# Performance work log

Hardware: AMD Instinct MI355X
Metric: run time of the kernel (lower is better)

Reference implementation:

```python
import jax, jax.numpy as jnp
import numpy as np

ALPHA = 1.0
EPS = 1e-12  # tf.nn.l2_normalize epsilon


def setup_inputs() -> dict:
    key = jax.random.key(0)
    k1, k2 = jax.random.split(key)
    B, I, J, D, K = 32, 32, 32, 128, 64
    features = jax.random.normal(k1, (B, I, J, D), dtype=jnp.float32)
    kmeans_centers = jax.random.normal(k2, (B, K, D), dtype=jnp.float32)
    return {"features": features, "kmeans_centers": kmeans_centers}


def reference(features, kmeans_centers):
    # features: (B, I, J, D); kmeans_centers: (B, K, D)
    B = features.shape[0]
    # Squared distance ||f - c||^2 expanded to avoid materializing (B,I,J,K,D)
    f2 = jnp.sum(features * features, axis=-1)[..., None]          # (B,I,J,1)
    c2 = jnp.sum(kmeans_centers * kmeans_centers, axis=-1)[:, None, None, :]  # (B,1,1,K)
    fc = jnp.einsum('bijd,bkd->bijk', features, kmeans_centers)     # (B,I,J,K)
    d2 = f2 - 2.0 * fc + c2                                         # (B,I,J,K)
    sim = jax.nn.softmax(-ALPHA * d2, axis=-1)                      # (B,I,J,K)
    # vlad[b,k,d] = sum_ij sim[b,i,j,k] * (f[b,i,j,d] - c[b,k,d])
    vlad = (jnp.einsum('bijk,bijd->bkd', sim, features)
            - jnp.sum(sim, axis=(1, 2))[..., None] * kmeans_centers)  # (B,K,D)
    flat = vlad.reshape(B, -1)                                      # (B, K*D)
    # K.l2_normalize with axis=None -> normalize over ALL elements (global norm)
    norm = jnp.sqrt(jnp.maximum(jnp.sum(flat * flat), EPS))
    return flat / norm
```

## Files before the change

kernel.cpp:

```cpp
#include <hip/hip_runtime.h>


#define NB    32
#define NIJ   1024
#define ND    128
#define NK    64
#define SPLIT 16
#define PPB   64

typedef short short8 __attribute__((ext_vector_type(8)));
typedef float f32x4  __attribute__((ext_vector_type(4)));

__device__ __forceinline__ float bf2f(unsigned short u) {
    return __uint_as_float(((unsigned)u) << 16);
}
__device__ __forceinline__ unsigned short f2bf(float f) {
    unsigned u = __float_as_uint(f);
    return (unsigned short)((u + 0x7fffu + ((u >> 16) & 1u)) >> 16);
}

__global__ __launch_bounds__(256, 2)
void netvlad_main(const float* __restrict__ feat,
                  const float* __restrict__ cent,
                  float* __restrict__ partial)
{
    __shared__ __align__(16) char smem[81920];
    ushort4* centHi = (ushort4*)smem;
    ushort4* centLo = (ushort4*)(smem + 16384);
    float4*  fL     = (float4*)(smem + 32768);
    float*   simf   = (float*)(smem + 65536);
    float4*  sim4   = (float4*)(smem + 65536);

    const int tid = threadIdx.x;
    const int bs  = blockIdx.x;
    const int b   = bs >> 4;
    const int n0  = (bs & 15) * PPB;

    const float4* cent4 = (const float4*)cent + (size_t)b * (NK * ND / 4);
    const float4* feat4 = (const float4*)feat + ((size_t)b * NIJ + n0) * (ND / 4);

    #pragma unroll
    for (int it = 0; it < 8; ++it) {
        int g  = it * 256 + tid;
        int k  = g >> 5;
        int d4 = g & 31;
        float4 v = cent4[g];
        ushort4 h, l;
        h.x = f2bf(v.x); l.x = f2bf(v.x - bf2f(h.x));
        h.y = f2bf(v.y); l.y = f2bf(v.y - bf2f(h.y));
        h.z = f2bf(v.z); l.z = f2bf(v.z - bf2f(h.z));
        h.w = f2bf(v.w); l.w = f2bf(v.w - bf2f(h.w));
        int idx = k * 32 + (d4 ^ ((k & 7) << 1));
        centHi[idx] = h; centLo[idx] = l;
    }
    #pragma unroll
    for (int it = 0; it < 8; ++it) {
        int g  = it * 256 + tid;
        int p  = g >> 5;
        int d4 = g & 31;
        fL[p * 32 + (d4 ^ (p & 7))] = feat4[g];
    }
    __syncthreads();

    if (tid < NK) {
        int k = tid;
        float a = 0.f;
        #pragma unroll
        for (int d4 = 0; d4 < 32; ++d4) {
            int idx = k * 32 + (d4 ^ ((k & 7) << 1));
            ushort4 h = centHi[idx], l = centLo[idx];
            float c0 = bf2f(h.x) + bf2f(l.x);
            float c1 = bf2f(h.y) + bf2f(l.y);
            float c2v = bf2f(h.z) + bf2f(l.z);
            float c3 = bf2f(h.w) + bf2f(l.w);
            a += c0 * c0 + c1 * c1 + c2v * c2v + c3 * c3;
        }
        simf[k] = a;
    }
    __syncthreads();

    const int w  = tid >> 6;
    const int l  = tid & 63;
    const int lr = l & 15;
    const int lg = l >> 4;

    float c2r[4];
    #pragma unroll
    for (int nt = 0; nt < 4; ++nt) c2r[nt] = simf[nt * 16 + lr];
    __syncthreads();

    f32x4 acc[4];
    #pragma unroll
    for (int nt = 0; nt < 4; ++nt) acc[nt] = (f32x4){0.f, 0.f, 0.f, 0.f};

    const int prow = 16 * w + lr;
    #pragma unroll
    for (int kt = 0; kt < 4; ++kt) {
        float4 fa = fL[prow * 32 + ((kt * 8 + 2 * lg + 0) ^ (prow & 7))];
        float4 fb = fL[prow * 32 + ((kt * 8 + 2 * lg + 1) ^ (prow & 7))];
        float fv[8] = { fa.x, fa.y, fa.z, fa.w, fb.x, fb.y, fb.z, fb.w };
        short8 ah, al;
        #pragma unroll
        for (int j = 0; j < 8; ++j) {
            unsigned short h = f2bf(fv[j]);
            ah[j] = (short)h;
            al[j] = (short)f2bf(fv[j] - bf2f(h));
        }
        #pragma unroll
        for (int nt = 0; nt < 4; ++nt) {
            int c  = nt * 16 + lr;
            int ch = c * 16 + ((kt * 4 + lg) ^ (c & 7));
            short8 bh = *(const short8*)(smem + ch * 16);
            short8 bl = *(const short8*)(smem + 16384 + ch * 16);
            acc[nt] = __builtin_amdgcn_mfma_f32_16x16x32_bf16(ah, bh, acc[nt], 0, 0, 0);
            acc[nt] = __builtin_amdgcn_mfma_f32_16x16x32_bf16(ah, bl, acc[nt], 0, 0, 0);
            acc[nt] = __builtin_amdgcn_mfma_f32_16x16x32_bf16(al, bh, acc[nt], 0, 0, 0);
        }
    }

    #pragma unroll
    for (int r = 0; r < 4; ++r) {
        float s[4];
        #pragma unroll
        for (int nt = 0; nt < 4; ++nt) s[nt] = 2.f * acc[nt][r] - c2r[nt];
        float m = fmaxf(fmaxf(s[0], s[1]), fmaxf(s[2], s[3]));
        #pragma unroll
        for (int o = 8; o >= 1; o >>= 1) m = fmaxf(m, __shfl_xor(m, o));
        float e[4], t = 0.f;
        #pragma unroll
        for (int nt = 0; nt < 4; ++nt) { e[nt] = __expf(s[nt] - m); t += e[nt]; }
        #pragma unroll
        for (int o = 8; o >= 1; o >>= 1) t += __shfl_xor(t, o);
        float inv = __builtin_amdgcn_rcpf(t);
        int p = 16 * w + 4 * lg + r;
        #pragma unroll
        for (int nt = 0; nt < 4; ++nt) {
            int k  = nt * 16 + lr;
            int kc = k >> 2;
            int slot = (((kc >> 2) ^ ((p >> 2) & 3)) << 2) | ((kc & 3) ^ (p & 3));
            simf[p * 64 + slot * 4 + (k & 3)] = e[nt] * inv;
        }
    }
    __syncthreads();

    const int kg = tid >> 5;
    const int dg = tid & 31;
    float4 a2[8];
    float  ss[8];
    #pragma unroll
    for (int i = 0; i < 8; ++i) { a2[i] = make_float4(0.f, 0.f, 0.f, 0.f); ss[i] = 0.f; }

    const int kcq = kg >> 1;
    const int kl0 = 2 * (kg & 1);
    #pragma unroll 4
    for (int p = 0; p < 64; ++p) {
        float4 fv = fL[p * 32 + (dg ^ (p & 7))];
        int pz2 = (p >> 2) & 3, pz = p & 3;
        int s0 = (((kcq ^ pz2) << 2) | ((kl0 + 0) ^ pz));
        int s1 = (((kcq ^ pz2) << 2) | ((kl0 + 1) ^ pz));
        float4 sa = sim4[p * 16 + s0];
        float4 sb = sim4[p * 16 + s1];
        float sv[8] = { sa.x, sa.y, sa.z, sa.w, sb.x, sb.y, sb.z, sb.w };
        #pragma unroll
        for (int i = 0; i < 8; ++i) {
            a2[i].x += sv[i] * fv.x;
            a2[i].y += sv[i] * fv.y;
            a2[i].z += sv[i] * fv.z;
            a2[i].w += sv[i] * fv.w;
            ss[i]   += sv[i];
        }
    }

    float4* out4 = (float4*)partial + (size_t)bs * (NK * ND / 4);
    #pragma unroll
    for (int i = 0; i < 8; ++i) {
        int k   = kg * 8 + i;
        int idx = k * 32 + (dg ^ ((k & 7) << 1));
        ushort4 h = centHi[idx], lo = centLo[idx];
        float4 o;
        o.x = a2[i].x - ss[i] * (bf2f(h.x) + bf2f(lo.x));
        o.y = a2[i].y - ss[i] * (bf2f(h.y) + bf2f(lo.y));
        o.z = a2[i].z - ss[i] * (bf2f(h.z) + bf2f(lo.z));
        o.w = a2[i].w - ss[i] * (bf2f(h.w) + bf2f(lo.w));
        out4[k * 32 + dg] = o;
    }
}

__global__ __launch_bounds__(256)
void netvlad_reduce(const float* __restrict__ partial,
                    float* __restrict__ vlad,
                    float* __restrict__ sqpart) {
    __shared__ float wsum[4];
    int idx = blockIdx.x * 256 + threadIdx.x;
    int b   = idx >> 11;
    int r   = idx & 2047;
    const float4* p4 = (const float4*)partial;
    float4 a = make_float4(0.f, 0.f, 0.f, 0.f);
    #pragma unroll
    for (int s = 0; s < SPLIT; ++s) {
        float4 v = p4[((size_t)(b * SPLIT + s)) * 2048 + r];
        a.x += v.x; a.y += v.y; a.z += v.z; a.w += v.w;
    }
    ((float4*)vlad)[idx] = a;
    float sq = a.x * a.x + a.y * a.y + a.z * a.z + a.w * a.w;
    #pragma unroll
    for (int o = 32; o >= 1; o >>= 1) sq += __shfl_xor(sq, o);
    if ((threadIdx.x & 63) == 0) wsum[threadIdx.x >> 6] = sq;
    __syncthreads();
    if (threadIdx.x == 0) sqpart[blockIdx.x] = wsum[0] + wsum[1] + wsum[2] + wsum[3];
}

__global__ __launch_bounds__(256)
void netvlad_norm(const float* __restrict__ vlad,
                  const float* __restrict__ sqpart,
                  float* __restrict__ out) {
    const float4* sq4 = (const float4*)sqpart;
    float4 v = sq4[threadIdx.x & 63];
    float t = v.x + v.y + v.z + v.w;
    #pragma unroll
    for (int o = 32; o >= 1; o >>= 1) t += __shfl_xor(t, o);
    float inv = __builtin_amdgcn_rcpf(sqrtf(fmaxf(t, 1e-12f)));
    int idx = blockIdx.x * 256 + threadIdx.x;
    float4 x = ((const float4*)vlad)[idx];
    float4 o4 = make_float4(x.x * inv, x.y * inv, x.z * inv, x.w * inv);
    ((float4*)out)[idx] = o4;
}

extern "C" void kernel_launch(void* const* d_in, const int* in_sizes, int n_in,
                              void* d_out, int out_size, void* d_ws, size_t ws_size,
                              hipStream_t stream) {
    const float* feat = (const float*)d_in[0];
    const float* cent = (const float*)d_in[1];
    float* out = (float*)d_out;

    char* ws = (char*)d_ws;
    const size_t partial_bytes = (size_t)NB * SPLIT * NK * ND * sizeof(float);
    const size_t vlad_bytes    = (size_t)NB * NK * ND * sizeof(float);
    float* partial = (float*)ws;
    float* vlad    = (float*)(ws + partial_bytes);
    float* sqpart  = (float*)(ws + partial_bytes + vlad_bytes);

    netvlad_main  <<<NB * SPLIT, 256, 0, stream>>>(feat, cent, partial);
    netvlad_reduce<<<256, 256, 0, stream>>>(partial, vlad, sqpart);
    netvlad_norm  <<<256, 256, 0, stream>>>(vlad, sqpart, out);
}
```

Measured before the change: 85.56 us.

## Compute VLAD aggregation with bf16 MFMA and move centre subtraction to reduce

The second contraction (sim^T × features) moves from scalar FP32 FMAs to bf16 MFMA, using transposed, swizzled bf16 copies of the features and similarities in LDS. Features are loaded straight from global into registers for the first MFMA instead of going through an FP32 LDS tile, which cuts shared memory to allow more occupancy. Per-split similarity sums are written to a new global buffer, and the reduce kernel subtracts ssum*centre. The cost is lower precision in the aggregation, since both operands are single bf16 with no hi/lo split.

```diff
diff --git a/kernel.cpp b/kernel.cpp
--- a/kernel.cpp
+++ b/kernel.cpp
@@ -2,11 +2,7 @@
 
 
 #define NB    32
-#define NIJ   1024
-#define ND    128
-#define NK    64
 #define SPLIT 16
-#define PPB   64
 
 typedef short short8 __attribute__((ext_vector_type(8)));
 typedef float f32x4  __attribute__((ext_vector_type(4)));
@@ -18,26 +14,29 @@
     unsigned u = __float_as_uint(f);
     return (unsigned short)((u + 0x7fffu + ((u >> 16) & 1u)) >> 16);
 }
+__device__ __forceinline__ int swz3(int x) { return (x ^ (x >> 3)) & 7; }
 
 __global__ __launch_bounds__(256, 2)
 void netvlad_main(const float* __restrict__ feat,
                   const float* __restrict__ cent,
-                  float* __restrict__ partial)
+                  float* __restrict__ partial,
+                  float* __restrict__ ssumG)
 {
-    __shared__ __align__(16) char smem[81920];
-    ushort4* centHi = (ushort4*)smem;
-    ushort4* centLo = (ushort4*)(smem + 16384);
-    float4*  fL     = (float4*)(smem + 32768);
-    float*   simf   = (float*)(smem + 65536);
-    float4*  sim4   = (float4*)(smem + 65536);
+    __shared__ __align__(16) char smem[58624];
+    ushort4*        centHi = (ushort4*)smem;
+    ushort4*        centLo = (ushort4*)(smem + 16384);
+    unsigned short* FT     = (unsigned short*)(smem + 32768);
+    unsigned short* ST     = (unsigned short*)(smem + 49152);
+    float*          c2L    = (float*)(smem + 57344);
+    float*          ssumW  = (float*)(smem + 57600);
 
     const int tid = threadIdx.x;
     const int bs  = blockIdx.x;
     const int b   = bs >> 4;
-    const int n0  = (bs & 15) * PPB;
-
-    const float4* cent4 = (const float4*)cent + (size_t)b * (NK * ND / 4);
-    const float4* feat4 = (const float4*)feat + ((size_t)b * NIJ + n0) * (ND / 4);
+    const int n0  = (bs & 15) * 64;
+
+    const float4* cent4 = (const float4*)cent + (size_t)b * 2048;
+    const float4* feat4 = (const float4*)feat + ((size_t)b * 1024 + n0) * 32;
 
     #pragma unroll
     for (int it = 0; it < 8; ++it) {
@@ -53,16 +52,31 @@
         int idx = k * 32 + (d4 ^ ((k & 7) << 1));
         centHi[idx] = h; centLo[idx] = l;
     }
-    #pragma unroll
-    for (int it = 0; it < 8; ++it) {
-        int g  = it * 256 + tid;
-        int p  = g >> 5;
-        int d4 = g & 31;
-        fL[p * 32 + (d4 ^ (p & 7))] = feat4[g];
-    }
-    __syncthreads();
-
-    if (tid < NK) {
+
+    const int w    = tid >> 6;
+    const int lane = tid & 63;
+    const int lr   = lane & 15;
+    const int lg   = lane >> 4;
+    const int prow = 16 * w + lr;
+
+    short8 ah[4], al[4];
+    #pragma unroll
+    for (int kt = 0; kt < 4; ++kt) {
+        float4 fa = feat4[prow * 32 + kt * 8 + 2 * lg + 0];
+        float4 fb = feat4[prow * 32 + kt * 8 + 2 * lg + 1];
+        float fv[8] = { fa.x, fa.y, fa.z, fa.w, fb.x, fb.y, fb.z, fb.w };
+        #pragma unroll
+        for (int j = 0; j < 8; ++j) {
+            unsigned short h = f2bf(fv[j]);
+            ah[kt][j] = (short)h;
+            al[kt][j] = (short)f2bf(fv[j] - bf2f(h));
+            int d = kt * 32 + 8 * lg + j;
+            FT[d * 64 + ((((prow >> 3) ^ swz3(d))) << 3) + (prow & 7)] = h;
+        }
+    }
+    __syncthreads();
+
+    if (tid < 64) {
         int k = tid;
         float a = 0.f;
         #pragma unroll
@@ -75,49 +89,32 @@
             float c3 = bf2f(h.w) + bf2f(l.w);
             a += c0 * c0 + c1 * c1 + c2v * c2v + c3 * c3;
         }
-        simf[k] = a;
-    }
-    __syncthreads();
-
-    const int w  = tid >> 6;
-    const int l  = tid & 63;
-    const int lr = l & 15;
-    const int lg = l >> 4;
+        c2L[k] = a;
+    }
+    __syncthreads();
 
     float c2r[4];
     #pragma unroll
-    for (int nt = 0; nt < 4; ++nt) c2r[nt] = simf[nt * 16 + lr];
-    __syncthreads();
+    for (int nt = 0; nt < 4; ++nt) c2r[nt] = c2L[nt * 16 + lr];
 
     f32x4 acc[4];
     #pragma unroll
     for (int nt = 0; nt < 4; ++nt) acc[nt] = (f32x4){0.f, 0.f, 0.f, 0.f};
-
-    const int prow = 16 * w + lr;
     #pragma unroll
     for (int kt = 0; kt < 4; ++kt) {
-        float4 fa = fL[prow * 32 + ((kt * 8 + 2 * lg + 0) ^ (prow & 7))];
-        float4 fb = fL[prow * 32 + ((kt * 8 + 2 * lg + 1) ^ (prow & 7))];
-        float fv[8] = { fa.x, fa.y, fa.z, fa.w, fb.x, fb.y, fb.z, fb.w };
-        short8 ah, al;
-        #pragma unroll
-        for (int j = 0; j < 8; ++j) {
-            unsigned short h = f2bf(fv[j]);
-            ah[j] = (short)h;
-            al[j] = (short)f2bf(fv[j] - bf2f(h));
-        }
         #pragma unroll
         for (int nt = 0; nt < 4; ++nt) {
             int c  = nt * 16 + lr;
             int ch = c * 16 + ((kt * 4 + lg) ^ (c & 7));
             short8 bh = *(const short8*)(smem + ch * 16);
             short8 bl = *(const short8*)(smem + 16384 + ch * 16);
-            acc[nt] = __builtin_amdgcn_mfma_f32_16x16x32_bf16(ah, bh, acc[nt], 0, 0, 0);
-            acc[nt] = __builtin_amdgcn_mfma_f32_16x16x32_bf16(ah, bl, acc[nt], 0, 0, 0);
-            acc[nt] = __builtin_amdgcn_mfma_f32_16x16x32_bf16(al, bh, acc[nt], 0, 0, 0);
-        }
-    }
-
+            acc[nt] = __builtin_amdgcn_mfma_f32_16x16x32_bf16(ah[kt], bh, acc[nt], 0, 0, 0);
+            acc[nt] = __builtin_amdgcn_mfma_f32_16x16x32_bf16(ah[kt], bl, acc[nt], 0, 0, 0);
+            acc[nt] = __builtin_amdgcn_mfma_f32_16x16x32_bf16(al[kt], bh, acc[nt], 0, 0, 0);
+        }
+    }
+
+    float ssp[4] = {0.f, 0.f, 0.f, 0.f};
     #pragma unroll
     for (int r = 0; r < 4; ++r) {
         float s[4];
@@ -135,72 +132,73 @@
         int p = 16 * w + 4 * lg + r;
         #pragma unroll
         for (int nt = 0; nt < 4; ++nt) {
-            int k  = nt * 16 + lr;
-            int kc = k >> 2;
-            int slot = (((kc >> 2) ^ ((p >> 2) & 3)) << 2) | ((kc & 3) ^ (p & 3));
-            simf[p * 64 + slot * 4 + (k & 3)] = e[nt] * inv;
-        }
-    }
-    __syncthreads();
-
-    const int kg = tid >> 5;
-    const int dg = tid & 31;
-    float4 a2[8];
-    float  ss[8];
-    #pragma unroll
-    for (int i = 0; i < 8; ++i) { a2[i] = make_float4(0.f, 0.f, 0.f, 0.f); ss[i] = 0.f; }
-
-    const int kcq = kg >> 1;
-    const int kl0 = 2 * (kg & 1);
-    #pragma unroll 4
-    for (int p = 0; p < 64; ++p) {
-        float4 fv = fL[p * 32 + (dg ^ (p & 7))];
-        int pz2 = (p >> 2) & 3, pz = p & 3;
-        int s0 = (((kcq ^ pz2) << 2) | ((kl0 + 0) ^ pz));
-        int s1 = (((kcq ^ pz2) << 2) | ((kl0 + 1) ^ pz));
-        float4 sa = sim4[p * 16 + s0];
-        float4 sb = sim4[p * 16 + s1];
-        float sv[8] = { sa.x, sa.y, sa.z, sa.w, sb.x, sb.y, sb.z, sb.w };
-        #pragma unroll
-        for (int i = 0; i < 8; ++i) {
-            a2[i].x += sv[i] * fv.x;
-            a2[i].y += sv[i] * fv.y;
-            a2[i].z += sv[i] * fv.z;
-            a2[i].w += sv[i] * fv.w;
-            ss[i]   += sv[i];
-        }
-    }
-
-    float4* out4 = (float4*)partial + (size_t)bs * (NK * ND / 4);
-    #pragma unroll
-    for (int i = 0; i < 8; ++i) {
-        int k   = kg * 8 + i;
-        int idx = k * 32 + (dg ^ ((k & 7) << 1));
-        ushort4 h = centHi[idx], lo = centLo[idx];
-        float4 o;
-        o.x = a2[i].x - ss[i] * (bf2f(h.x) + bf2f(lo.x));
-        o.y = a2[i].y - ss[i] * (bf2f(h.y) + bf2f(lo.y));
-        o.z = a2[i].z - ss[i] * (bf2f(h.z) + bf2f(lo.z));
-        o.w = a2[i].w - ss[i] * (bf2f(h.w) + bf2f(lo.w));
-        out4[k * 32 + dg] = o;
+            int k = nt * 16 + lr;
+            float val = e[nt] * inv;
+            ssp[nt] += val;
+            ST[k * 64 + ((((p >> 3) ^ swz3(k))) << 3) + (p & 7)] = f2bf(val);
+        }
+    }
+    #pragma unroll
+    for (int nt = 0; nt < 4; ++nt) {
+        float v = ssp[nt];
+        v += __shfl_xor(v, 16);
+        v += __shfl_xor(v, 32);
+        if (lg == 0) ssumW[w * 64 + nt * 16 + lr] = v;
+    }
+    __syncthreads();
+
+    if (tid < 64)
+        ssumG[bs * 64 + tid] = ssumW[tid] + ssumW[64 + tid] + ssumW[128 + tid] + ssumW[192 + tid];
+
+    f32x4 vac[8];
+    #pragma unroll
+    for (int dt = 0; dt < 8; ++dt) vac[dt] = (f32x4){0.f, 0.f, 0.f, 0.f};
+    const int krow = 16 * w + lr;
+    #pragma unroll
+    for (int ks = 0; ks < 2; ++ks) {
+        int cA = (ks * 4 + lg) ^ swz3(krow);
+        short8 af = *(const short8*)(ST + krow * 64 + (cA << 3));
+        #pragma unroll
+        for (int dt = 0; dt < 8; ++dt) {
+            int d  = dt * 16 + lr;
+            int cB = (ks * 4 + lg) ^ swz3(d);
+            short8 bf = *(const short8*)(FT + d * 64 + (cB << 3));
+            vac[dt] = __builtin_amdgcn_mfma_f32_16x16x32_bf16(af, bf, vac[dt], 0, 0, 0);
+        }
+    }
+
+    float* outp = partial + (size_t)bs * 8192;
+    #pragma unroll
+    for (int r = 0; r < 4; ++r) {
+        int k = 16 * w + 4 * lg + r;
+        #pragma unroll
+        for (int dt = 0; dt < 8; ++dt)
+            outp[k * 128 + dt * 16 + lr] = vac[dt][r];
     }
 }
 
 __global__ __launch_bounds__(256)
 void netvlad_reduce(const float* __restrict__ partial,
+                    const float* __restrict__ cent,
+                    const float* __restrict__ ssumG,
                     float* __restrict__ vlad,
                     float* __restrict__ sqpart) {
     __shared__ float wsum[4];
     int idx = blockIdx.x * 256 + threadIdx.x;
     int b   = idx >> 11;
-    int r   = idx & 2047;
+    int rem = idx & 2047;
+    int k   = rem >> 5;
     const float4* p4 = (const float4*)partial;
     float4 a = make_float4(0.f, 0.f, 0.f, 0.f);
+    float  ss = 0.f;
     #pragma unroll
     for (int s = 0; s < SPLIT; ++s) {
-        float4 v = p4[((size_t)(b * SPLIT + s)) * 2048 + r];
+        float4 v = p4[((size_t)(b * SPLIT + s)) * 2048 + rem];
         a.x += v.x; a.y += v.y; a.z += v.z; a.w += v.w;
-    }
+        ss += ssumG[(b * SPLIT + s) * 64 + k];
+    }
+    float4 c4 = ((const float4*)cent)[b * 2048 + rem];
+    a.x -= ss * c4.x; a.y -= ss * c4.y; a.z -= ss * c4.z; a.w -= ss * c4.w;
     ((float4*)vlad)[idx] = a;
     float sq = a.x * a.x + a.y * a.y + a.z * a.z + a.w * a.w;
     #pragma unroll
@@ -222,8 +220,7 @@
     float inv = __builtin_amdgcn_rcpf(sqrtf(fmaxf(t, 1e-12f)));
     int idx = blockIdx.x * 256 + threadIdx.x;
     float4 x = ((const float4*)vlad)[idx];
-    float4 o4 = make_float4(x.x * inv, x.y * inv, x.z * inv, x.w * inv);
-    ((float4*)out)[idx] = o4;
+    ((float4*)out)[idx] = make_float4(x.x * inv, x.y * inv, x.z * inv, x.w * inv);
 }
 
 extern "C" void kernel_launch(void* const* d_in, const int* in_sizes, int n_in,
@@ -234,13 +231,15 @@
     float* out = (float*)d_out;
 
     char* ws = (char*)d_ws;
-    const size_t partial_bytes = (size_t)NB * SPLIT * NK * ND * sizeof(float);
-    const size_t vlad_bytes    = (size_t)NB * NK * ND * sizeof(float);
+    const size_t partial_bytes = (size_t)NB * SPLIT * 64 * 128 * sizeof(float);
+    const size_t vlad_bytes    = (size_t)NB * 64 * 128 * sizeof(float);
+    const size_t ssum_bytes    = (size_t)NB * SPLIT * 64 * sizeof(float);
     float* partial = (float*)ws;
     float* vlad    = (float*)(ws + partial_bytes);
-    float* sqpart  = (float*)(ws + partial_bytes + vlad_bytes);
-
-    netvlad_main  <<<NB * SPLIT, 256, 0, stream>>>(feat, cent, partial);
-    netvlad_reduce<<<256, 256, 0, stream>>>(partial, vlad, sqpart);
+    float* ssumG   = (float*)(ws + partial_bytes + vlad_bytes);
+    float* sqpart  = (float*)(ws + partial_bytes + vlad_bytes + ssum_bytes);
+
+    netvlad_main  <<<NB * SPLIT, 256, 0, stream>>>(feat, cent, partial, ssumG);
+    netvlad_reduce<<<256, 256, 0, stream>>>(partial, cent, ssumG, vlad, sqpart);
     netvlad_norm  <<<256, 256, 0, stream>>>(vlad, sqpart, out);
 }
```

After: 79.23 us. 1.08x faster.
